# Kernel optimization log

Measured on AMD Instinct MI355X. Metric: run time of the kernel, lower is better.

Reference implementation:

```python
import jax, jax.numpy as jnp
import numpy as np

B, T, C = 4, 2048, 1024
H = 16
DH = C // H
DFF = 4 * C


def _layernorm(x, g, b, eps=1e-5):
    mu = jnp.mean(x, axis=-1, keepdims=True)
    var = jnp.var(x, axis=-1, keepdims=True)
    return (x - mu) * jax.lax.rsqrt(var + eps) * g + b


def setup_inputs() -> dict:
    key = jax.random.key(0)
    ks = jax.random.split(key, 12)
    s = 0.02
    return {
        "x": jax.random.normal(ks[0], (B, T, C), jnp.float32),
        "Wq": jax.random.normal(ks[1], (H, C, DH), jnp.float32) * s,
        "bq": jnp.zeros((H, DH), jnp.float32),
        "Wk": jax.random.normal(ks[2], (H, C, DH), jnp.float32) * s,
        "bk": jnp.zeros((H, DH), jnp.float32),
        "Wv": jax.random.normal(ks[3], (H, C, DH), jnp.float32) * s,
        "bv": jnp.zeros((H, DH), jnp.float32),
        "Wo": jax.random.normal(ks[4], (C, C), jnp.float32) * s,
        "bo": jnp.zeros((C,), jnp.float32),
        "ln1_g": jnp.ones((C,), jnp.float32),
        "ln1_b": jnp.zeros((C,), jnp.float32),
        "ln2_g": jnp.ones((C,), jnp.float32),
        "ln2_b": jnp.zeros((C,), jnp.float32),
        "W1": jax.random.normal(ks[5], (C, DFF), jnp.float32) * s,
        "b1": jnp.zeros((DFF,), jnp.float32),
        "W2": jax.random.normal(ks[6], (DFF, C), jnp.float32) * s,
        "b2": jnp.zeros((C,), jnp.float32),
    }


def reference(x, Wq, bq, Wk, bk, Wv, bv, Wo, bo, ln1_g, ln1_b, ln2_g, ln2_b, W1, b1, W2, b2):
    # pre-norm for attention
    xn = _layernorm(x, ln1_g, ln1_b)
    # per-head projections, batched: [B,H,T,DH]
    q = jnp.einsum("btc,hcd->bhtd", xn, Wq) + bq[None, :, None, :]
    k = jnp.einsum("btc,hcd->bhtd", xn, Wk) + bk[None, :, None, :]
    v = jnp.einsum("btc,hcd->bhtd", xn, Wv) + bv[None, :, None, :]
    # FAITHFUL to source: scores / scale with scale = DH**-0.5, i.e. * sqrt(DH)
    scores = jnp.einsum("bhtd,bhsd->bhts", q, k) * jnp.sqrt(jnp.float32(DH))
    attn = jax.nn.softmax(scores, axis=-1)
    o = jnp.einsum("bhts,bhsd->bhtd", attn, v)  # [B,H,T,DH]
    # concat heads along last dim (head order matches ModuleList concat)
    o = jnp.transpose(o, (0, 2, 1, 3)).reshape(B, T, C)
    attn_out = o @ Wo + bo  # dropout is identity at eval
    x = x + attn_out
    xn2 = _layernorm(x, ln2_g, ln2_b)
    ffn = jax.nn.relu(xn2 @ W1 + b1) @ W2 + b2
    return x + ffn
```

## Files before the change

### kernel.cpp

```cpp
#include <hip/hip_runtime.h>
#include <hip/hip_bf16.h>
#include <stdint.h>

typedef unsigned short ushort_t;
typedef short short8 __attribute__((ext_vector_type(8)));
typedef unsigned short ushortx8 __attribute__((ext_vector_type(8)));
typedef float floatx4 __attribute__((ext_vector_type(4)));

__device__ __forceinline__ float b2f(ushort_t u) {
    return __uint_as_float(((unsigned int)u) << 16);
}
__device__ __forceinline__ ushort_t f2bf(float f) {
    unsigned int u = __float_as_uint(f);
    unsigned int r = u + 0x7FFFu + ((u >> 16) & 1u);
    return (ushort_t)(r >> 16);
}
__device__ __forceinline__ unsigned int pack2bf(float a, float b) {
    return (unsigned int)f2bf(a) | ((unsigned int)f2bf(b) << 16);
}
__device__ __forceinline__ void gll16(const void* g, void* l) {
    __builtin_amdgcn_global_load_lds((const __attribute__((address_space(1))) unsigned int*)g,
                                     (__attribute__((address_space(3))) unsigned int*)l,
                                     16, 0, 0);
}

__global__ void transpose_kernel(const float* __restrict__ in, ushort_t* __restrict__ out,
                                 int K, int N) {
    __shared__ float tile[32][33];
    in += (long)blockIdx.z * K * N;
    out += (long)blockIdx.z * K * N;
    int k0 = blockIdx.x * 32, n0 = blockIdx.y * 32;
    int x = threadIdx.x, y = threadIdx.y;
#pragma unroll
    for (int i = 0; i < 4; i++)
        tile[y + 8 * i][x] = in[(long)(k0 + y + 8 * i) * N + n0 + x];
    __syncthreads();
#pragma unroll
    for (int i = 0; i < 4; i++)
        out[(long)(n0 + y + 8 * i) * K + k0 + x] = f2bf(tile[x][y + 8 * i]);
}

__global__ void concat_bias_kernel(const float* __restrict__ bq, const float* __restrict__ bk,
                                   const float* __restrict__ bv, float* __restrict__ dst) {
    int i = blockIdx.x * 256 + threadIdx.x;
    dst[i] = i < 1024 ? bq[i] : (i < 2048 ? bk[i - 1024] : bv[i - 2048]);
}

__global__ __launch_bounds__(256) void ln_kernel(const float* __restrict__ in,
                                                 ushort_t* __restrict__ out,
                                                 const float* __restrict__ g,
                                                 const float* __restrict__ b) {
    long row = blockIdx.x;
    int tid = threadIdx.x;
    float4 v4 = *((const float4*)(in + row * 1024) + tid);
    float v[4] = {v4.x, v4.y, v4.z, v4.w};
    float s1 = v[0] + v[1] + v[2] + v[3];
    float s2 = v[0] * v[0] + v[1] * v[1] + v[2] * v[2] + v[3] * v[3];
#pragma unroll
    for (int m = 32; m >= 1; m >>= 1) {
        s1 += __shfl_xor(s1, m);
        s2 += __shfl_xor(s2, m);
    }
    __shared__ float r1[4], r2[4];
    int w = tid >> 6;
    if ((tid & 63) == 0) { r1[w] = s1; r2[w] = s2; }
    __syncthreads();
    s1 = r1[0] + r1[1] + r1[2] + r1[3];
    s2 = r2[0] + r2[1] + r2[2] + r2[3];
    float mu = s1 * (1.0f / 1024.0f);
    float var = s2 * (1.0f / 1024.0f) - mu * mu;
    float inv = rsqrtf(var + 1e-5f);
    float y[4];
#pragma unroll
    for (int i = 0; i < 4; i++)
        y[i] = (v[i] - mu) * inv * g[tid * 4 + i] + b[tid * 4 + i];
    unsigned int lo = (unsigned int)f2bf(y[0]) | ((unsigned int)f2bf(y[1]) << 16);
    unsigned int hi = (unsigned int)f2bf(y[2]) | ((unsigned int)f2bf(y[3]) << 16);
    *(uint2*)(out + row * 1024 + tid * 4) = make_uint2(lo, hi);
}

template <typename OutT, int RELU, int MODE>
__device__ __forceinline__ void gemm128(
    const ushort_t* __restrict__ A, int lda,
    const ushort_t* __restrict__ Bt, int ldb, int K,
    OutT* __restrict__ C, long cBatch, int ldc,
    const float* __restrict__ bias, const float* __restrict__ resid,
    ushort_t* As, ushort_t* Bs) {
    int m0 = blockIdx.x * 128, n0 = blockIdx.y * 128;
    int tid = threadIdx.x, lane = tid & 63, w = tid >> 6;
    int ln = lane & 15, quad = lane >> 4;
    int wr = w >> 1, wc = w & 1;
    int lr = lane >> 2, lc = (lane & 3) * 8;

    auto stage = [&](int k0, int buf) {
#pragma unroll
        for (int i = 0; i < 4; i++) {
            int id = w * 4 + i;
            int blk = id & 7;
            int row = blk * 16 + lr;
            if (id < 8)
                gll16(A + (long)(m0 + row) * lda + k0 + lc, As + buf * 4096 + blk * 512);
            else
                gll16(Bt + (long)(n0 + row) * ldb + k0 + lc, Bs + buf * 4096 + blk * 512);
        }
    };

    floatx4 acc[4][4];
#pragma unroll
    for (int a = 0; a < 4; a++)
#pragma unroll
        for (int bb = 0; bb < 4; bb++) acc[a][bb] = floatx4{0, 0, 0, 0};

    stage(0, 0);
    int cur = 0;
    for (int k0 = 0; k0 < K; k0 += 32, cur ^= 1) {
        __syncthreads();
        if (k0 + 32 < K) stage(k0 + 32, cur ^ 1);
        const ushort_t* Ab = As + cur * 4096;
        const ushort_t* Bb = Bs + cur * 4096;
        short8 af[4], bf[4];
#pragma unroll
        for (int j = 0; j < 4; j++) {
            af[j] = *(const short8*)(Ab + (wr * 64 + j * 16 + ln) * 32 + quad * 8);
            bf[j] = *(const short8*)(Bb + (wc * 64 + j * 16 + ln) * 32 + quad * 8);
        }
#pragma unroll
        for (int a = 0; a < 4; a++)
#pragma unroll
            for (int bb = 0; bb < 4; bb++)
                acc[a][bb] = __builtin_amdgcn_mfma_f32_16x16x32_bf16(af[a], bf[bb], acc[a][bb], 0, 0, 0);
    }
#pragma unroll
    for (int bb = 0; bb < 4; bb++) {
        int gn = n0 + wc * 64 + bb * 16 + ln;
        float bv = bias ? bias[gn] : 0.0f;
#pragma unroll
        for (int a = 0; a < 4; a++) {
#pragma unroll
            for (int r = 0; r < 4; r++) {
                int gm = m0 + wr * 64 + a * 16 + quad * 4 + r;
                float val = acc[a][bb][r] + bv;
                if (RELU) val = fmaxf(val, 0.0f);
                if constexpr (MODE == 2) {
                    int gnl = gn & 1023;
                    long off;
                    if (gn < 2048)
                        off = (long)(gn >> 10) * 8388608 + (long)(gm >> 11) * 2097152 +
                              (long)(gm & 2047) * 1024 + gnl;
                    else
                        off = 16777216L +
                              ((((long)(gm >> 11)) * 16 + (gnl >> 6)) * 64 + (gnl & 63)) * 2048 +
                              (gm & 2047);
                    C[off] = (OutT)f2bf(val);
                } else {
                    long off = (long)(gm >> 11) * cBatch + (long)(gm & 2047) * ldc + gn;
                    if (resid) val += resid[off];
                    if constexpr (sizeof(OutT) == 2)
                        C[off] = (OutT)f2bf(val);
                    else
                        C[off] = (OutT)val;
                }
            }
        }
    }
}

__global__ __launch_bounds__(256) void gemm128_qkv_kernel(
    const ushort_t* __restrict__ A, const ushort_t* __restrict__ Bt,
    ushort_t* __restrict__ C, const float* __restrict__ bias) {
    __shared__ ushort_t As[2 * 128 * 32];
    __shared__ ushort_t Bs[2 * 128 * 32];
    gemm128<ushort_t, 0, 2>(A, 1024, Bt, 1024, 1024, C, 0, 0, bias, nullptr, As, Bs);
}

__global__ __launch_bounds__(256) void gemm128_bf16_relu_kernel(
    const ushort_t* __restrict__ A, int lda, const ushort_t* __restrict__ Bt, int ldb, int K,
    ushort_t* __restrict__ C, long cBatch, int ldc, const float* __restrict__ bias) {
    __shared__ ushort_t As[2 * 128 * 32];
    __shared__ ushort_t Bs[2 * 128 * 32];
    gemm128<ushort_t, 1, 0>(A, lda, Bt, ldb, K, C, cBatch, ldc, bias, nullptr, As, Bs);
}

__global__ __launch_bounds__(256) void gemm128_f32_kernel(
    const ushort_t* __restrict__ A, int lda, const ushort_t* __restrict__ Bt, int ldb, int K,
    float* __restrict__ C, long cBatch, int ldc,
    const float* __restrict__ bias, const float* __restrict__ resid) {
    __shared__ ushort_t As[2 * 128 * 32];
    __shared__ ushort_t Bs[2 * 128 * 32];
    gemm128<float, 0, 0>(A, lda, Bt, ldb, K, C, cBatch, ldc, bias, resid, As, Bs);
}

__global__ __launch_bounds__(512, 4) void attn_kernel(
    const ushort_t* __restrict__ q, const ushort_t* __restrict__ k,
    const ushort_t* __restrict__ vt, ushort_t* __restrict__ o) {
    __shared__ ushort_t Klds[2 * 4096];
    __shared__ ushort_t Vlds[2 * 4096];
    __shared__ ushort_t Plds[8 * 32 * 64];
    int flat = blockIdx.x;
    int bh = (flat & 7) * 8 + (flat >> 6);
    int xt = (flat >> 3) & 7;
    int b = bh >> 4, h = bh & 15;
    int t0 = xt * 256;
    int tid = threadIdx.x, lane = tid & 63, w = tid >> 6;
    int ln = lane & 15, quad = lane >> 4;
    int lr = lane >> 2, lq = lane & 3;
    int bsrc = (lane & 48) + ((lane >> 4) << 2);
    int rsw = (ln >> 1) & 3;
    int ssw = (lr >> 1) & 3;
    int p7 = ln & 7;

    const ushort_t* qbase = q + ((long)b * 2048 + t0 + w * 32) * 1024 + h * 64;
    short8 qf[2][2];
#pragma unroll
    for (int sub = 0; sub < 2; sub++)
#pragma unroll
        for (int s = 0; s < 2; s++) {
            ushortx8 t = *(const ushortx8*)(qbase + (long)(sub * 16 + ln) * 1024 + s * 32 + quad * 8);
#pragma unroll
            for (int j = 0; j < 8; j++) qf[sub][s][j] = (short)f2bf(b2f(t[j]) * 8.0f);
        }

    floatx4 O[2][4];
    float m_i[2] = {-1e30f, -1e30f}, l_i[2] = {0.0f, 0.0f};
#pragma unroll
    for (int sub = 0; sub < 2; sub++)
#pragma unroll
        for (int i = 0; i < 4; i++) O[sub][i] = floatx4{0, 0, 0, 0};

    ushort_t* Pw = Plds + w * 32 * 64;
    long krow0 = (long)b * 2048 * 1024 + h * 64;
    const ushort_t* vbase = vt + (long)bh * 64 * 2048;

    auto stage = [&](int kv0, int buf) {
#pragma unroll
        for (int i = 0; i < 2; i++) {
            int id = w * 2 + i;
            int s = (id >> 2) & 1, qt = id & 3;
            int row = qt * 16 + lr;
            int cs = ((lq ^ ssw) << 3);
            if (id < 8)
                gll16(k + krow0 + (long)(kv0 + row) * 1024 + s * 32 + cs,
                      Klds + buf * 4096 + s * 2048 + qt * 512);
            else
                gll16(vbase + (long)row * 2048 + kv0 + s * 32 + cs,
                      Vlds + buf * 4096 + s * 2048 + qt * 512);
        }
    };

    stage(0, 0);
    int cur = 0;
    for (int t32 = 0; t32 < 32; t32++, cur ^= 1) {
        __syncthreads();
        if (t32 < 31) stage((t32 + 1) * 64, cur ^ 1);
        const ushort_t* Kb = Klds + cur * 4096;
        const ushort_t* Vb = Vlds + cur * 4096;

        floatx4 Z[2][4];
#pragma unroll
        for (int sub = 0; sub < 2; sub++)
#pragma unroll
            for (int nc = 0; nc < 4; nc++) Z[sub][nc] = floatx4{0, 0, 0, 0};
#pragma unroll
        for (int s = 0; s < 2; s++)
#pragma unroll
            for (int nc = 0; nc < 4; nc++) {
                short8 kf = *(const short8*)(Kb + s * 2048 + (nc * 16 + ln) * 32 + ((quad ^ rsw) << 3));
                Z[0][nc] = __builtin_amdgcn_mfma_f32_16x16x32_bf16(kf, qf[0][s], Z[0][nc], 0, 0, 0);
                Z[1][nc] = __builtin_amdgcn_mfma_f32_16x16x32_bf16(kf, qf[1][s], Z[1][nc], 0, 0, 0);
            }

        float alpha[2];
#pragma unroll
        for (int sub = 0; sub < 2; sub++) {
            float mx = -1e30f;
#pragma unroll
            for (int nc = 0; nc < 4; nc++)
#pragma unroll
                for (int r = 0; r < 4; r++) mx = fmaxf(mx, Z[sub][nc][r]);
            mx = fmaxf(mx, __shfl_xor(mx, 16));
            mx = fmaxf(mx, __shfl_xor(mx, 32));
            float nm = fmaxf(m_i[sub], mx);
            alpha[sub] = __expf(m_i[sub] - nm);
            m_i[sub] = nm;
            float rs = 0.0f;
            ushort_t* Ps = Pw + (sub * 16 + ln) * 64;
#pragma unroll
            for (int nc = 0; nc < 4; nc++) {
                float p0 = __expf(Z[sub][nc][0] - nm), p1 = __expf(Z[sub][nc][1] - nm);
                float p2 = __expf(Z[sub][nc][2] - nm), p3 = __expf(Z[sub][nc][3] - nm);
                rs += (p0 + p1) + (p2 + p3);
                int col = (((nc * 2 + (quad >> 1)) ^ p7) << 3) | ((quad & 1) << 2);
                *(uint2*)(Ps + col) = make_uint2(pack2bf(p0, p1), pack2bf(p2, p3));
            }
            rs += __shfl_xor(rs, 16);
            rs += __shfl_xor(rs, 32);
            l_i[sub] = l_i[sub] * alpha[sub] + rs;
        }
#pragma unroll
        for (int sub = 0; sub < 2; sub++)
#pragma unroll
            for (int r = 0; r < 4; r++) {
                float ar = __shfl(alpha[sub], bsrc + r);
#pragma unroll
                for (int dc = 0; dc < 4; dc++) O[sub][dc][r] *= ar;
            }
        short8 pf[2][2];
#pragma unroll
        for (int sub = 0; sub < 2; sub++)
#pragma unroll
            for (int s = 0; s < 2; s++)
                pf[sub][s] = *(const short8*)(Pw + (sub * 16 + ln) * 64 +
                                              ((((s << 2) + quad) ^ p7) << 3));
#pragma unroll
        for (int s = 0; s < 2; s++)
#pragma unroll
            for (int dc = 0; dc < 4; dc++) {
                short8 vf = *(const short8*)(Vb + s * 2048 + (dc * 16 + ln) * 32 + ((quad ^ rsw) << 3));
                O[0][dc] = __builtin_amdgcn_mfma_f32_16x16x32_bf16(pf[0][s], vf, O[0][dc], 0, 0, 0);
                O[1][dc] = __builtin_amdgcn_mfma_f32_16x16x32_bf16(pf[1][s], vf, O[1][dc], 0, 0, 0);
            }
    }
#pragma unroll
    for (int sub = 0; sub < 2; sub++)
#pragma unroll
        for (int r = 0; r < 4; r++) {
            float inv = 1.0f / __shfl(l_i[sub], bsrc + r);
            int t = t0 + w * 32 + sub * 16 + quad * 4 + r;
            ushort_t* orow = o + ((long)b * 2048 + t) * 1024 + h * 64;
#pragma unroll
            for (int dc = 0; dc < 4; dc++) orow[dc * 16 + ln] = f2bf(O[sub][dc][r] * inv);
        }
}

extern "C" void kernel_launch(void* const* d_in, const int* in_sizes, int n_in,
                              void* d_out, int out_size, void* d_ws, size_t ws_size,
                              hipStream_t stream) {
    const float* x   = (const float*)d_in[0];
    const float* Wq  = (const float*)d_in[1];
    const float* bq  = (const float*)d_in[2];
    const float* Wk  = (const float*)d_in[3];
    const float* bk  = (const float*)d_in[4];
    const float* Wv  = (const float*)d_in[5];
    const float* bv  = (const float*)d_in[6];
    const float* Wo  = (const float*)d_in[7];
    const float* bo  = (const float*)d_in[8];
    const float* g1  = (const float*)d_in[9];
    const float* be1 = (const float*)d_in[10];
    const float* g2  = (const float*)d_in[11];
    const float* be2 = (const float*)d_in[12];
    const float* W1  = (const float*)d_in[13];
    const float* b1  = (const float*)d_in[14];
    const float* W2  = (const float*)d_in[15];
    const float* b2  = (const float*)d_in[16];
    float* out = (float*)d_out;

    const long MB = 1 << 20;
    char* w = (char*)d_ws;
    ushort_t* xn  = (ushort_t*)(w);
    float*    x2  = (float*)(w + 16 * MB);
    ushort_t* qb  = (ushort_t*)(w + 48 * MB);
    ushort_t* kb  = (ushort_t*)(w + 64 * MB);
    ushort_t* vtb = (ushort_t*)(w + 80 * MB);
    ushort_t* xn2 = qb;
    ushort_t* h1  = (ushort_t*)(w + 64 * MB);
    ushort_t* WqT = (ushort_t*)(w + 96 * MB);
    ushort_t* WkT = (ushort_t*)(w + 98 * MB);
    ushort_t* WvT = (ushort_t*)(w + 100 * MB);
    ushort_t* WoT = (ushort_t*)(w + 102 * MB);
    ushort_t* W1T = (ushort_t*)(w + 104 * MB);
    ushort_t* W2T = (ushort_t*)(w + 112 * MB);
    float* biasCat = x2;

    dim3 tb(32, 8);
    transpose_kernel<<<dim3(32, 2, 16), tb, 0, stream>>>(Wq, WqT, 1024, 64);
    transpose_kernel<<<dim3(32, 2, 16), tb, 0, stream>>>(Wk, WkT, 1024, 64);
    transpose_kernel<<<dim3(32, 2, 16), tb, 0, stream>>>(Wv, WvT, 1024, 64);
    transpose_kernel<<<dim3(32, 32, 1), tb, 0, stream>>>(Wo, WoT, 1024, 1024);
    transpose_kernel<<<dim3(32, 128, 1), tb, 0, stream>>>(W1, W1T, 1024, 4096);
    transpose_kernel<<<dim3(128, 32, 1), tb, 0, stream>>>(W2, W2T, 4096, 1024);
    concat_bias_kernel<<<12, 256, 0, stream>>>(bq, bk, bv, biasCat);

    ln_kernel<<<8192, 256, 0, stream>>>(x, xn, g1, be1);
    gemm128_qkv_kernel<<<dim3(64, 24), 256, 0, stream>>>(xn, WqT, qb, biasCat);
    attn_kernel<<<512, 512, 0, stream>>>(qb, kb, vtb, xn );
    gemm128_f32_kernel<<<dim3(64, 8), 256, 0, stream>>>(xn, 1024, WoT, 1024, 1024,
                                                        x2, 2048L * 1024, 1024, bo, x);
    ln_kernel<<<8192, 256, 0, stream>>>((const float*)x2, xn2, g2, be2);
    gemm128_bf16_relu_kernel<<<dim3(64, 16), 256, 0, stream>>>(
        xn2, 1024, W1T, 1024, 1024, h1, 2048L * 2048, 2048, b1);
    gemm128_f32_kernel<<<dim3(64, 8), 256, 0, stream>>>(
        h1, 2048, W2T, 4096, 2048, out, 2048L * 1024, 1024, b2, x2);
    gemm128_bf16_relu_kernel<<<dim3(64, 16), 256, 0, stream>>>(
        xn2, 1024, W1T + 2048L * 1024, 1024, 1024, h1, 2048L * 2048, 2048, b1 + 2048);
    gemm128_f32_kernel<<<dim3(64, 8), 256, 0, stream>>>(
        h1, 2048, W2T + 2048, 4096, 2048, out, 2048L * 1024, 1024, nullptr, out);
}
```

Baseline: 599.4 us.

## Keep attention P in registers by permuting K rows, drop LDS roundtrip

The flash-attention kernel no longer writes the softmax probabilities to shared memory and reads them back in MFMA operand layout. Instead, K rows are loaded into LDS in a permuted order so the QK^T accumulator layout already matches the A-operand layout needed for the PV MFMA, and P is packed straight into registers. It also uses the hardware v_cvt_pk_bf16_f32 instruction for the bf16 packing. This removes LDS traffic and a per-warp P buffer, which may raise occupancy. The risk is correctness if the row permutation does not match the MFMA k-index mapping.

```diff
diff --git a/kernel.cpp b/kernel.cpp
--- a/kernel.cpp
+++ b/kernel.cpp
@@ -15,8 +15,10 @@
     unsigned int r = u + 0x7FFFu + ((u >> 16) & 1u);
     return (ushort_t)(r >> 16);
 }
-__device__ __forceinline__ unsigned int pack2bf(float a, float b) {
-    return (unsigned int)f2bf(a) | ((unsigned int)f2bf(b) << 16);
+__device__ __forceinline__ unsigned int cvtpk(float lo, float hi) {
+    unsigned int r;
+    asm("v_cvt_pk_bf16_f32 %0, %1, %2" : "=v"(r) : "v"(lo), "v"(hi));
+    return r;
 }
 __device__ __forceinline__ void gll16(const void* g, void* l) {
     __builtin_amdgcn_global_load_lds((const __attribute__((address_space(1))) unsigned int*)g,
@@ -195,7 +197,6 @@
     const ushort_t* __restrict__ vt, ushort_t* __restrict__ o) {
     __shared__ ushort_t Klds[2 * 4096];
     __shared__ ushort_t Vlds[2 * 4096];
-    __shared__ ushort_t Plds[8 * 32 * 64];
     int flat = blockIdx.x;
     int bh = (flat & 7) * 8 + (flat >> 6);
     int xt = (flat >> 3) & 7;
@@ -207,7 +208,6 @@
     int bsrc = (lane & 48) + ((lane >> 4) << 2);
     int rsw = (ln >> 1) & 3;
     int ssw = (lr >> 1) & 3;
-    int p7 = ln & 7;
 
     const ushort_t* qbase = q + ((long)b * 2048 + t0 + w * 32) * 1024 + h * 64;
     short8 qf[2][2];
@@ -227,7 +227,6 @@
 #pragma unroll
         for (int i = 0; i < 4; i++) O[sub][i] = floatx4{0, 0, 0, 0};
 
-    ushort_t* Pw = Plds + w * 32 * 64;
     long krow0 = (long)b * 2048 * 1024 + h * 64;
     const ushort_t* vbase = vt + (long)bh * 64 * 2048;
 
@@ -236,14 +235,16 @@
         for (int i = 0; i < 2; i++) {
             int id = w * 2 + i;
             int s = (id >> 2) & 1, qt = id & 3;
-            int row = qt * 16 + lr;
             int cs = ((lq ^ ssw) << 3);
-            if (id < 8)
-                gll16(k + krow0 + (long)(kv0 + row) * 1024 + s * 32 + cs,
+            if (id < 8) {
+                int prow = ((qt >> 1) << 5) + ((lr >> 2) << 3) + ((qt & 1) << 2) + (lr & 3);
+                gll16(k + krow0 + (long)(kv0 + prow) * 1024 + s * 32 + cs,
                       Klds + buf * 4096 + s * 2048 + qt * 512);
-            else
+            } else {
+                int row = qt * 16 + lr;
                 gll16(vbase + (long)row * 2048 + kv0 + s * 32 + cs,
                       Vlds + buf * 4096 + s * 2048 + qt * 512);
+            }
         }
     };
 
@@ -270,6 +271,7 @@
             }
 
         float alpha[2];
+        short8 pf[2][2];
 #pragma unroll
         for (int sub = 0; sub < 2; sub++) {
             float mx = -1e30f;
@@ -283,14 +285,19 @@
             alpha[sub] = __expf(m_i[sub] - nm);
             m_i[sub] = nm;
             float rs = 0.0f;
-            ushort_t* Ps = Pw + (sub * 16 + ln) * 64;
-#pragma unroll
-            for (int nc = 0; nc < 4; nc++) {
-                float p0 = __expf(Z[sub][nc][0] - nm), p1 = __expf(Z[sub][nc][1] - nm);
-                float p2 = __expf(Z[sub][nc][2] - nm), p3 = __expf(Z[sub][nc][3] - nm);
-                rs += (p0 + p1) + (p2 + p3);
-                int col = (((nc * 2 + (quad >> 1)) ^ p7) << 3) | ((quad & 1) << 2);
-                *(uint2*)(Ps + col) = make_uint2(pack2bf(p0, p1), pack2bf(p2, p3));
+#pragma unroll
+            for (int s = 0; s < 2; s++) {
+                float a0 = __expf(Z[sub][2 * s][0] - nm), a1 = __expf(Z[sub][2 * s][1] - nm);
+                float a2 = __expf(Z[sub][2 * s][2] - nm), a3 = __expf(Z[sub][2 * s][3] - nm);
+                float b0 = __expf(Z[sub][2 * s + 1][0] - nm), b1 = __expf(Z[sub][2 * s + 1][1] - nm);
+                float b2 = __expf(Z[sub][2 * s + 1][2] - nm), b3 = __expf(Z[sub][2 * s + 1][3] - nm);
+                rs += ((a0 + a1) + (a2 + a3)) + ((b0 + b1) + (b2 + b3));
+                union { unsigned int u[4]; short8 v; } pu;
+                pu.u[0] = cvtpk(a0, a1);
+                pu.u[1] = cvtpk(a2, a3);
+                pu.u[2] = cvtpk(b0, b1);
+                pu.u[3] = cvtpk(b2, b3);
+                pf[sub][s] = pu.v;
             }
             rs += __shfl_xor(rs, 16);
             rs += __shfl_xor(rs, 32);
@@ -304,13 +311,6 @@
 #pragma unroll
                 for (int dc = 0; dc < 4; dc++) O[sub][dc][r] *= ar;
             }
-        short8 pf[2][2];
-#pragma unroll
-        for (int sub = 0; sub < 2; sub++)
-#pragma unroll
-            for (int s = 0; s < 2; s++)
-                pf[sub][s] = *(const short8*)(Pw + (sub * 16 + ln) * 64 +
-                                              ((((s << 2) + quad) ^ p7) << 3));
 #pragma unroll
         for (int s = 0; s < 2; s++)
 #pragma unroll
```

Result: no change. 594.2 us (-0.9%).
